# Kernel tuning notes

Hardware: AMD Instinct MI355X
Metric: run time of the kernel (lower is better)

## Reference

```python
import jax, jax.numpy as jnp
import numpy as np

TEMP_EPS = 1e-6


def setup_inputs() -> dict:
    key = jax.random.key(0)
    k1, k2, k3 = jax.random.split(key, 3)
    B, V = 128, 128256
    logits = jax.random.normal(k1, (B, V), dtype=jnp.float32)
    temperatures = jax.random.uniform(k2, (B,), dtype=jnp.float32)
    u = jax.random.uniform(k3, (B, V), dtype=jnp.float32)
    return {"logits": logits, "temperatures": temperatures, "u": u}


def reference(logits, temperatures, u):
    # Faithful vectorized version of the per-row loop:
    #   nan_to_num -> temperature scale -> softmax -> multinomial sample,
    # expressed as a single Gumbel-max over the batch (equivalent sampling
    # distribution), with greedy argmax where temp <= 1e-6.
    logits = jnp.nan_to_num(logits)                       # [B, V]
    greedy = jnp.argmax(logits, axis=-1)                  # [B]

    safe_temp = jnp.maximum(temperatures, TEMP_EPS)[:, None]  # [B, 1]
    scaled = logits / safe_temp                           # [B, V]

    # Gumbel-max trick: argmax(scaled + g), g ~ Gumbel(0,1), samples
    # exactly from softmax(scaled) == the multinomial in the original.
    uc = jnp.clip(u, 1e-10, 1.0 - 1e-7)
    gumbel = -jnp.log(-jnp.log(uc))                       # [B, V]
    sampled = jnp.argmax(scaled + gumbel, axis=-1)        # [B]

    use_greedy = temperatures <= TEMP_EPS                 # [B] bool
    return jnp.where(use_greedy, greedy, sampled)
```

## Files before the change

### kernel.cpp

```cpp
#include <hip/hip_runtime.h>
#include <cfloat>
#include <cstdint>


#define TEMP_EPS 1e-6f

static constexpr int V       = 128256;
static constexpr int V4      = V / 4;
static constexpr int SEGS    = 32;
static constexpr int SEG_V4  = V4 / SEGS;
static constexpr int TAIL    = SEG_V4 - 3 * 256;

__device__ __forceinline__ float nan_to_num_f(float x) {
    if (x != x) return 0.0f;
    return fminf(fmaxf(x, -FLT_MAX), FLT_MAX);
}

__device__ __forceinline__ unsigned long long pack_key(float v, int idx) {
    unsigned b = __float_as_uint(v);
    unsigned mask = (unsigned)(((int)b >> 31)) | 0x80000000u;
    b ^= mask;
    return ((unsigned long long)b << 32) | (unsigned)(~(unsigned)idx);
}

__device__ __forceinline__ unsigned long long umax64(unsigned long long a,
                                                     unsigned long long b) {
    return a > b ? a : b;
}

__global__ __launch_bounds__(256) void sampler_partial_kernel(
    const float* __restrict__ logits,
    const float* __restrict__ temps,
    const float* __restrict__ u,
    unsigned long long* __restrict__ partials) {
    const int row = blockIdx.y;
    const int seg = blockIdx.x;
    const int tid = threadIdx.x;

    const float temp = temps[row];
    const bool greedy = (temp <= TEMP_EPS);
    const float safe_temp = fmaxf(temp, TEMP_EPS);

    const float4* __restrict__ l4 = (const float4*)(logits + (size_t)row * V);
    const float4* __restrict__ u4 = (const float4*)(u + (size_t)row * V);

    const float UC_LO = 1e-10f;
    const float UC_HI = (float)(1.0 - 1e-7);

    const int base = seg * SEG_V4;

    int idx[4];
    idx[0] = base + tid;
    idx[1] = base + 256 + tid;
    idx[2] = base + 512 + tid;
    idx[3] = (tid < TAIL) ? (base + 768 + tid) : (base + tid);

    float4 lv[4], uv[4];
#pragma unroll
    for (int k = 0; k < 4; ++k) lv[k] = l4[idx[k]];
#pragma unroll
    for (int k = 0; k < 4; ++k) uv[k] = u4[idx[k]];

    unsigned long long key = 0ULL;

    if (greedy) {
#pragma unroll
        for (int k = 0; k < 4; ++k) {
            const int e = idx[k] * 4;
            float a = nan_to_num_f(lv[k].x);
            float b = nan_to_num_f(lv[k].y);
            float c = nan_to_num_f(lv[k].z);
            float d = nan_to_num_f(lv[k].w);
            key = umax64(key, pack_key(a, e + 0));
            key = umax64(key, pack_key(b, e + 1));
            key = umax64(key, pack_key(c, e + 2));
            key = umax64(key, pack_key(d, e + 3));
        }
    } else {
#pragma unroll
        for (int k = 0; k < 4; ++k) {
            const int e = idx[k] * 4;

            float l0 = nan_to_num_f(lv[k].x) / safe_temp;
            float l1 = nan_to_num_f(lv[k].y) / safe_temp;
            float l2 = nan_to_num_f(lv[k].z) / safe_temp;
            float l3 = nan_to_num_f(lv[k].w) / safe_temp;

            float c0 = fminf(fmaxf(uv[k].x, UC_LO), UC_HI);
            float c1 = fminf(fmaxf(uv[k].y, UC_LO), UC_HI);
            float c2 = fminf(fmaxf(uv[k].z, UC_LO), UC_HI);
            float c3 = fminf(fmaxf(uv[k].w, UC_LO), UC_HI);

            float g0 = -logf(-logf(c0));
            float g1 = -logf(-logf(c1));
            float g2 = -logf(-logf(c2));
            float g3 = -logf(-logf(c3));

            key = umax64(key, pack_key(l0 + g0, e + 0));
            key = umax64(key, pack_key(l1 + g1, e + 1));
            key = umax64(key, pack_key(l2 + g2, e + 2));
            key = umax64(key, pack_key(l3 + g3, e + 3));
        }
    }

    for (int o = 32; o > 0; o >>= 1)
        key = umax64(key, __shfl_down(key, o));

    __shared__ unsigned long long sdata[4];
    if ((tid & 63) == 0) sdata[tid >> 6] = key;
    __syncthreads();

    if (tid == 0) {
        for (int w = 1; w < 4; ++w) key = umax64(key, sdata[w]);
        partials[row * SEGS + seg] = key;
    }
}

__global__ __launch_bounds__(64) void sampler_reduce_kernel(
    const unsigned long long* __restrict__ partials,
    int* __restrict__ out) {
    const int row = blockIdx.x;
    const int t = threadIdx.x;
    unsigned long long key = (t < SEGS) ? partials[row * SEGS + t] : 0ULL;
    for (int o = 32; o > 0; o >>= 1)
        key = umax64(key, __shfl_down(key, o));
    if (t == 0)
        out[row] = (int)(~(unsigned)(key & 0xFFFFFFFFull));
}

extern "C" void kernel_launch(void* const* d_in, const int* in_sizes, int n_in,
                              void* d_out, int out_size, void* d_ws, size_t ws_size,
                              hipStream_t stream) {
    const float* logits = (const float*)d_in[0];
    const float* temps  = (const float*)d_in[1];
    const float* u      = (const float*)d_in[2];
    int* out = (int*)d_out;
    const int B = in_sizes[1];

    unsigned long long* partials = (unsigned long long*)d_ws;

    dim3 grid1(SEGS, B);
    hipLaunchKernelGGL(sampler_partial_kernel, grid1, dim3(256), 0, stream,
                       logits, temps, u, partials);
    hipLaunchKernelGGL(sampler_reduce_kernel, dim3(B), dim3(64), 0, stream,
                       partials, out);
}
```

Measured before the change: 148.6 us.

## Use fast log approximations, reciprocal temperature, and skip u loads on greedy rows

Swaps logf for __logf with a polynomial path for u near 1, replaces the per-element division with a multiply by a precomputed reciprocal fused into an FMA, and drops the nan_to_num clamping. Greedy rows no longer load the u tensor, and each float4 group is reduced with float max before a single 64-bit key compare. This cuts transcendental and integer-compare ALU work and reads less memory for greedy rows. In exchange it changes rounding, since the fast log and reciprocal can flip near-tied argmax results, and NaN or inf inputs are no longer sanitized.

```diff
diff --git a/kernel.cpp b/kernel.cpp
--- a/kernel.cpp
+++ b/kernel.cpp
@@ -11,11 +11,6 @@
 static constexpr int SEG_V4  = V4 / SEGS;
 static constexpr int TAIL    = SEG_V4 - 3 * 256;
 
-__device__ __forceinline__ float nan_to_num_f(float x) {
-    if (x != x) return 0.0f;
-    return fminf(fmaxf(x, -FLT_MAX), FLT_MAX);
-}
-
 __device__ __forceinline__ unsigned long long pack_key(float v, int idx) {
     unsigned b = __float_as_uint(v);
     unsigned mask = (unsigned)(((int)b >> 31)) | 0x80000000u;
@@ -26,6 +21,19 @@
 __device__ __forceinline__ unsigned long long umax64(unsigned long long a,
                                                      unsigned long long b) {
     return a > b ? a : b;
+}
+
+__device__ __forceinline__ float neg_log_fast(float c) {
+    float t = c - 1.0f;
+    float p = -1.0f / 6.0f;
+    p = __builtin_fmaf(p, t, 0.2f);
+    p = __builtin_fmaf(p, t, -0.25f);
+    p = __builtin_fmaf(p, t, 1.0f / 3.0f);
+    p = __builtin_fmaf(p, t, -0.5f);
+    p = __builtin_fmaf(p, t, 1.0f);
+    float wpoly = -t * p;
+    float whw = -__logf(c);
+    return (c >= 0.90625f) ? wpoly : whw;
 }
 
 __global__ __launch_bounds__(256) void sampler_partial_kernel(
@@ -40,6 +48,7 @@
     const float temp = temps[row];
     const bool greedy = (temp <= TEMP_EPS);
     const float safe_temp = fmaxf(temp, TEMP_EPS);
+    const float inv_temp = 1.0f / safe_temp;
 
     const float4* __restrict__ l4 = (const float4*)(logits + (size_t)row * V);
     const float4* __restrict__ u4 = (const float4*)(u + (size_t)row * V);
@@ -55,51 +64,61 @@
     idx[2] = base + 512 + tid;
     idx[3] = (tid < TAIL) ? (base + 768 + tid) : (base + tid);
 
-    float4 lv[4], uv[4];
-#pragma unroll
-    for (int k = 0; k < 4; ++k) lv[k] = l4[idx[k]];
-#pragma unroll
-    for (int k = 0; k < 4; ++k) uv[k] = u4[idx[k]];
-
     unsigned long long key = 0ULL;
 
     if (greedy) {
+        float4 lv[4];
+#pragma unroll
+        for (int k = 0; k < 4; ++k) lv[k] = l4[idx[k]];
 #pragma unroll
         for (int k = 0; k < 4; ++k) {
             const int e = idx[k] * 4;
-            float a = nan_to_num_f(lv[k].x);
-            float b = nan_to_num_f(lv[k].y);
-            float c = nan_to_num_f(lv[k].z);
-            float d = nan_to_num_f(lv[k].w);
-            key = umax64(key, pack_key(a, e + 0));
-            key = umax64(key, pack_key(b, e + 1));
-            key = umax64(key, pack_key(c, e + 2));
-            key = umax64(key, pack_key(d, e + 3));
+            float m01 = fmaxf(lv[k].x, lv[k].y);
+            float m23 = fmaxf(lv[k].z, lv[k].w);
+            float m = fmaxf(m01, m23);
+            int ei = (lv[k].x == m) ? e
+                   : (lv[k].y == m) ? e + 1
+                   : (lv[k].z == m) ? e + 2 : e + 3;
+            key = umax64(key, pack_key(m, ei));
         }
     } else {
+        float4 lv[4], uv[4];
+#pragma unroll
+        for (int k = 0; k < 4; ++k) lv[k] = l4[idx[k]];
+#pragma unroll
+        for (int k = 0; k < 4; ++k) uv[k] = u4[idx[k]];
+
 #pragma unroll
         for (int k = 0; k < 4; ++k) {
             const int e = idx[k] * 4;
-
-            float l0 = nan_to_num_f(lv[k].x) / safe_temp;
-            float l1 = nan_to_num_f(lv[k].y) / safe_temp;
-            float l2 = nan_to_num_f(lv[k].z) / safe_temp;
-            float l3 = nan_to_num_f(lv[k].w) / safe_temp;
 
             float c0 = fminf(fmaxf(uv[k].x, UC_LO), UC_HI);
             float c1 = fminf(fmaxf(uv[k].y, UC_LO), UC_HI);
             float c2 = fminf(fmaxf(uv[k].z, UC_LO), UC_HI);
             float c3 = fminf(fmaxf(uv[k].w, UC_LO), UC_HI);
 
-            float g0 = -logf(-logf(c0));
-            float g1 = -logf(-logf(c1));
-            float g2 = -logf(-logf(c2));
-            float g3 = -logf(-logf(c3));
+            float w0 = neg_log_fast(c0);
+            float w1 = neg_log_fast(c1);
+            float w2 = neg_log_fast(c2);
+            float w3 = neg_log_fast(c3);
 
-            key = umax64(key, pack_key(l0 + g0, e + 0));
-            key = umax64(key, pack_key(l1 + g1, e + 1));
-            key = umax64(key, pack_key(l2 + g2, e + 2));
-            key = umax64(key, pack_key(l3 + g3, e + 3));
+            float g0 = -__logf(w0);
+            float g1 = -__logf(w1);
+            float g2 = -__logf(w2);
+            float g3 = -__logf(w3);
+
+            float v0 = __builtin_fmaf(lv[k].x, inv_temp, g0);
+            float v1 = __builtin_fmaf(lv[k].y, inv_temp, g1);
+            float v2 = __builtin_fmaf(lv[k].z, inv_temp, g2);
+            float v3 = __builtin_fmaf(lv[k].w, inv_temp, g3);
+
+            float m01 = fmaxf(v0, v1);
+            float m23 = fmaxf(v2, v3);
+            float m = fmaxf(m01, m23);
+            int ei = (v0 == m) ? e
+                   : (v1 == m) ? e + 1
+                   : (v2 == m) ? e + 2 : e + 3;
+            key = umax64(key, pack_key(m, ei));
         }
     }
 
```

New measurement: 145.7 us. Within noise of the previous version (-1.9%).
